# Kernel optimization log

Measured on AMD Instinct MI355X. Metric: run time of the kernel, lower is better.

## Reference

```python
import jax, jax.numpy as jnp
import numpy as np

B, S, D, H = 2, 2048, 512, 8
DK = D // H


def setup_inputs() -> dict:
    key = jax.random.key(0)
    ks = jax.random.split(key, 6)
    q = jax.random.normal(ks[0], (B, S, D), dtype=jnp.float32)
    k = jax.random.normal(ks[1], (B, S, D), dtype=jnp.float32)
    v = jax.random.normal(ks[2], (B, S, D), dtype=jnp.float32)
    mask = jax.random.randint(ks[3], (1, 1, S, S), 0, 2, dtype=jnp.int32)
    # nn.Linear weights [out, in]; scaled like torch default init
    Wq = jax.random.normal(ks[4], (D, D), dtype=jnp.float32) / np.sqrt(D)
    Wo = jax.random.normal(ks[5], (D, D), dtype=jnp.float32) / np.sqrt(D)
    return {"q": q, "k": k, "v": v, "mask": mask, "Wq": Wq, "Wo": Wo}


def _split_heads(x):
    # [B,S,D] -> [B,H,S,DK]
    return x.reshape(B, S, H, DK).transpose(0, 2, 1, 3)


def reference(q, k, v, mask, Wq, Wo):
    # NOTE: original module applies Wq to q, k AND v (faithful to source bug)
    query = _split_heads(q @ Wq.T)
    key_ = _split_heads(k @ Wq.T)
    value = _split_heads(v @ Wq.T)
    scores = jnp.einsum("bhqd,bhkd->bhqk", query, key_) / np.sqrt(DK).astype(np.float32)
    # original uses masked_fill_(mask==0, 1e-09) BEFORE softmax (not -inf)
    scores = jnp.where(mask == 0, jnp.float32(1e-9), scores)
    attn = jax.nn.softmax(scores, axis=-1)  # dropout p=0.0 -> identity
    x = jnp.einsum("bhqk,bhkd->bhqd", attn, value)
    x = x.transpose(0, 2, 1, 3).reshape(B, S, D)
    return x @ Wo.T
```

## Files before the change

kernel.cpp:

```cpp
#include <hip/hip_runtime.h>
#include <hip/hip_bf16.h>
#include <stdint.h>

#define S_LEN 2048
#define D_MOD 512
#define N_H   8
#define D_K   64

typedef short v8s __attribute__((ext_vector_type(8)));
typedef short v4s __attribute__((ext_vector_type(4)));
typedef float v4f __attribute__((ext_vector_type(4)));

__device__ __forceinline__ short f2bf(float f) {
  union { float f; unsigned u; } a; a.f = f;
  unsigned u = a.u;
  u += 0x7fffu + ((u >> 16) & 1u);
  return (short)(u >> 16);
}
__device__ __forceinline__ short f2bfh(float f) {
  union { float f; unsigned u; } a; a.f = f;
  return (short)((a.u + 0x8000u) >> 16);
}
__device__ __forceinline__ float bf2f(short s) {
  union { unsigned u; float f; } x;
  x.u = ((unsigned)(unsigned short)s) << 16;
  return x.f;
}

__device__ __forceinline__ v4f mfma16(v8s a, v8s b, v4f c) {
  return __builtin_amdgcn_mfma_f32_16x16x32_bf16(a, b, c, 0, 0, 0);
}
__device__ __forceinline__ v4f mfma16x16(v4s a, v4s b, v4f c) {
  return __builtin_amdgcn_mfma_f32_16x16x16bf16_1k(a, b, c, 0, 0, 0);
}

__global__ __launch_bounds__(256) void proj_kernel(
    const float* __restrict__ q, const float* __restrict__ k,
    const float* __restrict__ v, const float* __restrict__ Wq,
    const float* __restrict__ Wo, const int* __restrict__ mask,
    short* __restrict__ QP, short* __restrict__ KP, short* __restrict__ VT,
    short* __restrict__ Wob, unsigned long long* __restrict__ mp)
{
  const int z = blockIdx.z;
  const int tid = threadIdx.x;
  if (z == 3) {
    int bid = blockIdx.x * 8 + blockIdx.y;
    if (bid < 256) {
      int id = bid * 256 + tid;
      const int4* m4 = (const int4*)(mask + (size_t)id * 64);
      unsigned long long w = 0ull;
#pragma unroll
      for (int j = 0; j < 16; j++) {
        int4 mv = m4[j];
        w |= (unsigned long long)(mv.x != 0) << (j * 4 + 0);
        w |= (unsigned long long)(mv.y != 0) << (j * 4 + 1);
        w |= (unsigned long long)(mv.z != 0) << (j * 4 + 2);
        w |= (unsigned long long)(mv.w != 0) << (j * 4 + 3);
      }
      mp[id] = w;
    } else {
      unsigned off = (bid - 256) * 256 + tid;
      float4 x = ((const float4*)Wo)[off];
      v4s p; p.x = f2bf(x.x); p.y = f2bf(x.y); p.z = f2bf(x.z); p.w = f2bf(x.w);
      ((v4s*)Wob)[off] = p;
    }
    return;
  }
  const float* __restrict__ A = (z == 0) ? q : ((z == 1) ? k : v);
  const int m0 = blockIdx.x * 64, n0 = blockIdx.y * 64;
  const int wave = tid >> 6, lane = tid & 63;
  const int quad = lane >> 4, l15 = lane & 15;
  const int wm = wave >> 1, wn = wave & 1;
  __shared__ short As[64][72];
  __shared__ short Bs[64][72];
  v4f acc[2][2];
#pragma unroll
  for (int i = 0; i < 2; i++)
#pragma unroll
    for (int j = 0; j < 2; j++) acc[i][j] = (v4f){0.f, 0.f, 0.f, 0.f};

  float4 a4[4], b4[4];
#pragma unroll
  for (int i = 0; i < 4; i++) {
    int fi = tid + i * 256, r = fi >> 4, c = (fi & 15) << 2;
    a4[i] = *(const float4*)&A[(m0 + r) * 512 + c];
    b4[i] = *(const float4*)&Wq[(n0 + r) * 512 + c];
  }

  for (int kk = 0; kk < 512; kk += 64) {
    __syncthreads();
#pragma unroll
    for (int i = 0; i < 4; i++) {
      int fi = tid + i * 256, r = fi >> 4, c = (fi & 15) << 2;
      v4s ap; ap.x = f2bf(a4[i].x); ap.y = f2bf(a4[i].y); ap.z = f2bf(a4[i].z); ap.w = f2bf(a4[i].w);
      *(v4s*)&As[r][c] = ap;
      v4s bp; bp.x = f2bf(b4[i].x); bp.y = f2bf(b4[i].y); bp.z = f2bf(b4[i].z); bp.w = f2bf(b4[i].w);
      *(v4s*)&Bs[r][c] = bp;
    }
    __syncthreads();
    if (kk + 64 < 512) {
#pragma unroll
      for (int i = 0; i < 4; i++) {
        int fi = tid + i * 256, r = fi >> 4, c = (fi & 15) << 2;
        a4[i] = *(const float4*)&A[(m0 + r) * 512 + kk + 64 + c];
        b4[i] = *(const float4*)&Wq[(n0 + r) * 512 + kk + 64 + c];
      }
    }
#pragma unroll
    for (int ms = 0; ms < 2; ms++)
#pragma unroll
      for (int ns = 0; ns < 2; ns++)
#pragma unroll
        for (int ks = 0; ks < 2; ks++) {
          union { v8s v; v4s h2[2]; } a, bb;
          a.h2[0]  = *(const v4s*)&As[wm * 32 + ms * 16 + l15][ks * 32 + quad * 8];
          a.h2[1]  = *(const v4s*)&As[wm * 32 + ms * 16 + l15][ks * 32 + quad * 8 + 4];
          bb.h2[0] = *(const v4s*)&Bs[wn * 32 + ns * 16 + l15][ks * 32 + quad * 8];
          bb.h2[1] = *(const v4s*)&Bs[wn * 32 + ns * 16 + l15][ks * 32 + quad * 8 + 4];
          acc[ms][ns] = mfma16(a.v, bb.v, acc[ms][ns]);
        }
  }
#pragma unroll
  for (int ms = 0; ms < 2; ms++)
#pragma unroll
    for (int ns = 0; ns < 2; ns++) {
      int mb = m0 + wm * 32 + ms * 16 + quad * 4;
      int n  = n0 + wn * 32 + ns * 16 + l15;
      int bI = mb >> 11, s = mb & 2047, hh = n >> 6, dk = n & 63;
      if (z == 2) {
        v4s pv;
        pv.x = f2bf(acc[ms][ns][0]); pv.y = f2bf(acc[ms][ns][1]);
        pv.z = f2bf(acc[ms][ns][2]); pv.w = f2bf(acc[ms][ns][3]);
        *(v4s*)&VT[((bI * N_H + hh) * D_K + dk) * S_LEN + s] = pv;
      } else {
        short* dst = (z == 0) ? QP : KP;
#pragma unroll
        for (int r = 0; r < 4; r++)
          dst[((bI * N_H + hh) * S_LEN + (s + r)) * D_K + dk] = f2bf(acc[ms][ns][r]);
      }
    }
}

__global__ __launch_bounds__(512, 4) void attn_kernel(
    const short* __restrict__ QP, const short* __restrict__ KP,
    const short* __restrict__ VT, const unsigned long long* __restrict__ MP,
    short* __restrict__ XB, float* __restrict__ LP)
{
  const int bx = blockIdx.x;
  const int qt = bx & 15, qu = bx >> 4;
  const int h = blockIdx.y, b = blockIdx.z;
  const int tid = threadIdx.x;
  const int wave = tid >> 6, lane = tid & 63;
  const int quad = lane >> 4, l15 = lane & 15;
  const short* Qh = QP + ((b * N_H + h) * S_LEN) * D_K;
  const short* Kh = KP + ((b * N_H + h) * S_LEN) * D_K;
  const short* Vh = VT + ((b * N_H + h) * D_K) * S_LEN;

  __shared__ short Ks[2][64][72];
  __shared__ short Vs[2][64][72];

  const int qrow = qt * 128 + wave * 16;
  const int srow = tid >> 3;
  const int sc   = (tid & 7) * 8;
  const int ck0  = qu * 512;

  v8s aQ[2];
#pragma unroll
  for (int ks = 0; ks < 2; ks++)
    aQ[ks] = *(const v8s*)&Qh[(qrow + l15) * D_K + ks * 32 + quad * 8];

  const float C1 = 0.18033688011112042f;
  const float C2 = -11.541560327111707f;
  const v4s ONES4 = {16256, 16256, 16256, 16256};
  v4f accX[4], accL = (v4f){0.f, 0.f, 0.f, 0.f};
#pragma unroll
  for (int u = 0; u < 4; u++) accX[u] = (v4f){0.f, 0.f, 0.f, 0.f};

  v8s kr = *(const v8s*)&Kh[(ck0 + srow) * D_K + sc];
  v8s vr = *(const v8s*)&Vh[srow * S_LEN + ck0 + sc];
  *(v8s*)&Ks[0][srow][sc] = kr;
  *(v8s*)&Vs[0][srow][sc] = vr;
  unsigned long long mwc = MP[(qrow + l15) * 32 + qu * 8];
  unsigned long long mwn = 0ull;
  __syncthreads();

  for (int kt = 0; kt < 8; kt++) {
    const int cur = kt & 1;
    if (kt + 1 < 8) {
      const int c1 = ck0 + (kt + 1) * 64;
      kr = *(const v8s*)&Kh[(c1 + srow) * D_K + sc];
      vr = *(const v8s*)&Vh[srow * S_LEN + c1 + sc];
      mwn = MP[(qrow + l15) * 32 + qu * 8 + kt + 1];
    }

    v4s pa[4];
#pragma unroll
    for (int tp = 0; tp < 4; tp++) {
      v8s bK0 = *(const v8s*)&Ks[cur][tp * 16 + l15][quad * 8];
      v8s bK1 = *(const v8s*)&Ks[cur][tp * 16 + l15][32 + quad * 8];
      v4f s = mfma16(bK0, aQ[0], (v4f){0.f, 0.f, 0.f, 0.f});
      s = mfma16(bK1, aQ[1], s);
      unsigned mb = (unsigned)(mwc >> (tp * 16 + quad * 4));
      v4s pk;
#pragma unroll
      for (int r = 0; r < 4; r++) {
        float se = ((mb >> r) & 1u) ? s[r] : 0.0f;
        float p = __builtin_amdgcn_exp2f(fmaf(se, C1, C2));
        pk[r] = f2bfh(p);
      }
      pa[tp] = pk;
    }

#pragma unroll
    for (int u = 0; u < 4; u++) {
      const short* vb_ = &Vs[cur][u * 16 + l15][quad * 4];
#pragma unroll
      for (int tp = 0; tp < 4; tp++) {
        v4s bV = *(const v4s*)&vb_[tp * 16];
        accX[u] = mfma16x16(pa[tp], bV, accX[u]);
      }
    }
#pragma unroll
    for (int tp = 0; tp < 4; tp++)
      accL = mfma16x16(pa[tp], ONES4, accL);

    if (kt + 1 < 8) {
      *(v8s*)&Ks[cur ^ 1][srow][sc] = kr;
      *(v8s*)&Vs[cur ^ 1][srow][sc] = vr;
    }
    __syncthreads();
    mwc = mwn;
  }

  short* xq = XB + (size_t)qu * 2097152u;
#pragma unroll
  for (int u = 0; u < 4; u++)
#pragma unroll
    for (int r = 0; r < 4; r++) {
      int srw = qrow + quad * 4 + r;
      xq[(b * S_LEN + srw) * D_MOD + h * D_K + u * 16 + l15] = f2bf(accX[u][r]);
    }
  if (l15 == 0) {
#pragma unroll
    for (int r = 0; r < 4; r++) {
      int srw = qrow + quad * 4 + r;
      LP[((qu * 2 + b) * S_LEN + srw) * N_H + h] = accL[r];
    }
  }
}

__global__ __launch_bounds__(256) void outproj_kernel(
    const short* __restrict__ XB, const float* __restrict__ LP,
    const short* __restrict__ Wob, float* __restrict__ out)
{
  const int m0 = blockIdx.x * 64, n0 = blockIdx.y * 64;
  const int tid = threadIdx.x;
  const int wave = tid >> 6, lane = tid & 63;
  const int quad = lane >> 4, l15 = lane & 15;
  const int wm = wave >> 1, wn = wave & 1;
  __shared__ short As[64][72];
  __shared__ short Bs[64][72];
  __shared__ float Linv[64][8];

#pragma unroll
  for (int i = 0; i < 2; i++) {
    int e = tid + i * 256;
    int rr = e >> 3, hh = e & 7;
    int s = m0 + rr, bb = s >> 11, sl = s & 2047;
    float l = 0.f;
#pragma unroll
    for (int qu = 0; qu < 4; qu++)
      l += LP[((qu * 2 + bb) * S_LEN + sl) * N_H + hh];
    Linv[rr][hh] = 1.0f / l;
  }

  v4f acc[2][2];
#pragma unroll
  for (int i = 0; i < 2; i++)
#pragma unroll
    for (int j = 0; j < 2; j++) acc[i][j] = (v4f){0.f, 0.f, 0.f, 0.f};

  float af[2][8];
  v8s b8[2];
#pragma unroll
  for (int i = 0; i < 2; i++) {
    int fi = tid + i * 256, r = fi >> 3, c = (fi & 7) << 3;
    size_t base = (size_t)(m0 + r) * 512 + c;
#pragma unroll
    for (int j = 0; j < 8; j++) af[i][j] = 0.f;
#pragma unroll
    for (int qu = 0; qu < 4; qu++) {
      v8s t = *(const v8s*)(XB + (size_t)qu * 2097152u + base);
#pragma unroll
      for (int j = 0; j < 8; j++) af[i][j] += bf2f(t[j]);
    }
    b8[i] = *(const v8s*)&Wob[(n0 + r) * 512 + c];
  }
  __syncthreads();

  for (int kk = 0; kk < 512; kk += 64) {
#pragma unroll
    for (int i = 0; i < 2; i++) {
      int fi = tid + i * 256, r = fi >> 3, c = (fi & 7) << 3;
      float inv = Linv[r][kk >> 6];
      v8s ap;
#pragma unroll
      for (int j = 0; j < 8; j++) ap[j] = f2bf(af[i][j] * inv);
      *(v8s*)&As[r][c] = ap;
      *(v8s*)&Bs[r][c] = b8[i];
    }
    __syncthreads();
    if (kk + 64 < 512) {
#pragma unroll
      for (int i = 0; i < 2; i++) {
        int fi = tid + i * 256, r = fi >> 3, c = (fi & 7) << 3;
        size_t base = (size_t)(m0 + r) * 512 + kk + 64 + c;
#pragma unroll
        for (int j = 0; j < 8; j++) af[i][j] = 0.f;
#pragma unroll
        for (int qu = 0; qu < 4; qu++) {
          v8s t = *(const v8s*)(XB + (size_t)qu * 2097152u + base);
#pragma unroll
          for (int j = 0; j < 8; j++) af[i][j] += bf2f(t[j]);
        }
        b8[i] = *(const v8s*)&Wob[(n0 + r) * 512 + kk + 64 + c];
      }
    }
#pragma unroll
    for (int ms = 0; ms < 2; ms++)
#pragma unroll
      for (int ns = 0; ns < 2; ns++)
#pragma unroll
        for (int ks = 0; ks < 2; ks++) {
          union { v8s v; v4s h2[2]; } a, bb;
          a.h2[0]  = *(const v4s*)&As[wm * 32 + ms * 16 + l15][ks * 32 + quad * 8];
          a.h2[1]  = *(const v4s*)&As[wm * 32 + ms * 16 + l15][ks * 32 + quad * 8 + 4];
          bb.h2[0] = *(const v4s*)&Bs[wn * 32 + ns * 16 + l15][ks * 32 + quad * 8];
          bb.h2[1] = *(const v4s*)&Bs[wn * 32 + ns * 16 + l15][ks * 32 + quad * 8 + 4];
          acc[ms][ns] = mfma16(a.v, bb.v, acc[ms][ns]);
        }
    __syncthreads();
  }
#pragma unroll
  for (int ms = 0; ms < 2; ms++)
#pragma unroll
    for (int ns = 0; ns < 2; ns++) {
      int n = n0 + wn * 32 + ns * 16 + l15;
#pragma unroll
      for (int r = 0; r < 4; r++) {
        int m = m0 + wm * 32 + ms * 16 + quad * 4 + r;
        out[m * 512 + n] = acc[ms][ns][r];
      }
    }
}

extern "C" void kernel_launch(void* const* d_in, const int* in_sizes, int n_in,
                              void* d_out, int out_size, void* d_ws, size_t ws_size,
                              hipStream_t stream) {
  const float* q  = (const float*)d_in[0];
  const float* k  = (const float*)d_in[1];
  const float* v  = (const float*)d_in[2];
  const int* mask = (const int*)d_in[3];
  const float* Wq = (const float*)d_in[4];
  const float* Wo = (const float*)d_in[5];
  float* out = (float*)d_out;
  char* ws = (char*)d_ws;
  short* QP = (short*)(ws);
  short* KP = (short*)(ws + (4u << 20));
  short* VT = (short*)(ws + (8u << 20));
  unsigned long long* MP = (unsigned long long*)(ws + (16u << 20));
  short* Wob = (short*)(ws + (16u << 20) + (512u << 10));
  short* XB = (short*)(ws + (17u << 20));
  float* LP = (float*)(ws + (33u << 20));

  proj_kernel<<<dim3(64, 8, 4), 256, 0, stream>>>(q, k, v, Wq, Wo, mask,
                                                  QP, KP, VT, Wob, MP);
  attn_kernel<<<dim3(64, N_H, 2), 512, 0, stream>>>(QP, KP, VT, MP, XB, LP);
  outproj_kernel<<<dim3(64, 8, 1), 256, 0, stream>>>(XB, LP, Wob, out);
}
```

Baseline: 151.7 us.

## Drop split-K in attention and normalize rows inside the attention kernel

Removes the four-way key split across blocks. Each attention block now walks all 32 key tiles and normalizes its output by the row sum before writing bf16. This removes the partial-sum buffer, the extra XB traffic and the reduction plus rescale work in the output projection. In exchange the attention grid shrinks from 1024 to 256 blocks of 512 threads, which may leave the GPU's compute units underused.

```diff
diff --git a/kernel.cpp b/kernel.cpp
--- a/kernel.cpp
+++ b/kernel.cpp
@@ -144,10 +144,9 @@
 __global__ __launch_bounds__(512, 4) void attn_kernel(
     const short* __restrict__ QP, const short* __restrict__ KP,
     const short* __restrict__ VT, const unsigned long long* __restrict__ MP,
-    short* __restrict__ XB, float* __restrict__ LP)
+    short* __restrict__ XB)
 {
-  const int bx = blockIdx.x;
-  const int qt = bx & 15, qu = bx >> 4;
+  const int qt = blockIdx.x;
   const int h = blockIdx.y, b = blockIdx.z;
   const int tid = threadIdx.x;
   const int wave = tid >> 6, lane = tid & 63;
@@ -162,7 +161,6 @@
   const int qrow = qt * 128 + wave * 16;
   const int srow = tid >> 3;
   const int sc   = (tid & 7) * 8;
-  const int ck0  = qu * 512;
 
   v8s aQ[2];
 #pragma unroll
@@ -176,21 +174,21 @@
 #pragma unroll
   for (int u = 0; u < 4; u++) accX[u] = (v4f){0.f, 0.f, 0.f, 0.f};
 
-  v8s kr = *(const v8s*)&Kh[(ck0 + srow) * D_K + sc];
-  v8s vr = *(const v8s*)&Vh[srow * S_LEN + ck0 + sc];
+  v8s kr = *(const v8s*)&Kh[srow * D_K + sc];
+  v8s vr = *(const v8s*)&Vh[srow * S_LEN + sc];
   *(v8s*)&Ks[0][srow][sc] = kr;
   *(v8s*)&Vs[0][srow][sc] = vr;
-  unsigned long long mwc = MP[(qrow + l15) * 32 + qu * 8];
+  unsigned long long mwc = MP[(qrow + l15) * 32];
   unsigned long long mwn = 0ull;
   __syncthreads();
 
-  for (int kt = 0; kt < 8; kt++) {
+  for (int kt = 0; kt < 32; kt++) {
     const int cur = kt & 1;
-    if (kt + 1 < 8) {
-      const int c1 = ck0 + (kt + 1) * 64;
+    if (kt + 1 < 32) {
+      const int c1 = (kt + 1) * 64;
       kr = *(const v8s*)&Kh[(c1 + srow) * D_K + sc];
       vr = *(const v8s*)&Vh[srow * S_LEN + c1 + sc];
-      mwn = MP[(qrow + l15) * 32 + qu * 8 + kt + 1];
+      mwn = MP[(qrow + l15) * 32 + kt + 1];
     }
 
     v4s pa[4];
@@ -224,7 +222,7 @@
     for (int tp = 0; tp < 4; tp++)
       accL = mfma16x16(pa[tp], ONES4, accL);
 
-    if (kt + 1 < 8) {
+    if (kt + 1 < 32) {
       *(v8s*)&Ks[cur ^ 1][srow][sc] = kr;
       *(v8s*)&Vs[cur ^ 1][srow][sc] = vr;
     }
@@ -232,26 +230,22 @@
     mwc = mwn;
   }
 
-  short* xq = XB + (size_t)qu * 2097152u;
+  v4f linv;
+#pragma unroll
+  for (int r = 0; r < 4; r++) linv[r] = 1.0f / accL[r];
 #pragma unroll
   for (int u = 0; u < 4; u++)
 #pragma unroll
     for (int r = 0; r < 4; r++) {
       int srw = qrow + quad * 4 + r;
-      xq[(b * S_LEN + srw) * D_MOD + h * D_K + u * 16 + l15] = f2bf(accX[u][r]);
-    }
-  if (l15 == 0) {
-#pragma unroll
-    for (int r = 0; r < 4; r++) {
-      int srw = qrow + quad * 4 + r;
-      LP[((qu * 2 + b) * S_LEN + srw) * N_H + h] = accL[r];
-    }
-  }
+      XB[(b * S_LEN + srw) * D_MOD + h * D_K + u * 16 + l15] =
+          f2bf(accX[u][r] * linv[r]);
+    }
 }
 
 __global__ __launch_bounds__(256) void outproj_kernel(
-    const short* __restrict__ XB, const float* __restrict__ LP,
-    const short* __restrict__ Wob, float* __restrict__ out)
+    const short* __restrict__ XB, const short* __restrict__ Wob,
+    float* __restrict__ out)
 {
   const int m0 = blockIdx.x * 64, n0 = blockIdx.y * 64;
   const int tid = threadIdx.x;
@@ -260,19 +254,6 @@
   const int wm = wave >> 1, wn = wave & 1;
   __shared__ short As[64][72];
   __shared__ short Bs[64][72];
-  __shared__ float Linv[64][8];
-
-#pragma unroll
-  for (int i = 0; i < 2; i++) {
-    int e = tid + i * 256;
-    int rr = e >> 3, hh = e & 7;
-    int s = m0 + rr, bb = s >> 11, sl = s & 2047;
-    float l = 0.f;
-#pragma unroll
-    for (int qu = 0; qu < 4; qu++)
-      l += LP[((qu * 2 + bb) * S_LEN + sl) * N_H + hh];
-    Linv[rr][hh] = 1.0f / l;
-  }
 
   v4f acc[2][2];
 #pragma unroll
@@ -280,33 +261,20 @@
 #pragma unroll
     for (int j = 0; j < 2; j++) acc[i][j] = (v4f){0.f, 0.f, 0.f, 0.f};
 
-  float af[2][8];
-  v8s b8[2];
+  v8s a8[2], b8[2];
 #pragma unroll
   for (int i = 0; i < 2; i++) {
     int fi = tid + i * 256, r = fi >> 3, c = (fi & 7) << 3;
-    size_t base = (size_t)(m0 + r) * 512 + c;
-#pragma unroll
-    for (int j = 0; j < 8; j++) af[i][j] = 0.f;
-#pragma unroll
-    for (int qu = 0; qu < 4; qu++) {
-      v8s t = *(const v8s*)(XB + (size_t)qu * 2097152u + base);
-#pragma unroll
-      for (int j = 0; j < 8; j++) af[i][j] += bf2f(t[j]);
-    }
+    a8[i] = *(const v8s*)&XB[(m0 + r) * 512 + c];
     b8[i] = *(const v8s*)&Wob[(n0 + r) * 512 + c];
   }
-  __syncthreads();
 
   for (int kk = 0; kk < 512; kk += 64) {
+    __syncthreads();
 #pragma unroll
     for (int i = 0; i < 2; i++) {
       int fi = tid + i * 256, r = fi >> 3, c = (fi & 7) << 3;
-      float inv = Linv[r][kk >> 6];
-      v8s ap;
-#pragma unroll
-      for (int j = 0; j < 8; j++) ap[j] = f2bf(af[i][j] * inv);
-      *(v8s*)&As[r][c] = ap;
+      *(v8s*)&As[r][c] = a8[i];
       *(v8s*)&Bs[r][c] = b8[i];
     }
     __syncthreads();
@@ -314,15 +282,7 @@
 #pragma unroll
       for (int i = 0; i < 2; i++) {
         int fi = tid + i * 256, r = fi >> 3, c = (fi & 7) << 3;
-        size_t base = (size_t)(m0 + r) * 512 + kk + 64 + c;
-#pragma unroll
-        for (int j = 0; j < 8; j++) af[i][j] = 0.f;
-#pragma unroll
-        for (int qu = 0; qu < 4; qu++) {
-          v8s t = *(const v8s*)(XB + (size_t)qu * 2097152u + base);
-#pragma unroll
-          for (int j = 0; j < 8; j++) af[i][j] += bf2f(t[j]);
-        }
+        a8[i] = *(const v8s*)&XB[(m0 + r) * 512 + kk + 64 + c];
         b8[i] = *(const v8s*)&Wob[(n0 + r) * 512 + kk + 64 + c];
       }
     }
@@ -339,7 +299,6 @@
           bb.h2[1] = *(const v4s*)&Bs[wn * 32 + ns * 16 + l15][ks * 32 + quad * 8 + 4];
           acc[ms][ns] = mfma16(a.v, bb.v, acc[ms][ns]);
         }
-    __syncthreads();
   }
 #pragma unroll
   for (int ms = 0; ms < 2; ms++)
@@ -371,10 +330,9 @@
   unsigned long long* MP = (unsigned long long*)(ws + (16u << 20));
   short* Wob = (short*)(ws + (16u << 20) + (512u << 10));
   short* XB = (short*)(ws + (17u << 20));
-  float* LP = (float*)(ws + (33u << 20));
 
   proj_kernel<<<dim3(64, 8, 4), 256, 0, stream>>>(q, k, v, Wq, Wo, mask,
                                                   QP, KP, VT, Wob, MP);
-  attn_kernel<<<dim3(64, N_H, 2), 512, 0, stream>>>(QP, KP, VT, MP, XB, LP);
-  outproj_kernel<<<dim3(64, 8, 1), 256, 0, stream>>>(XB, LP, Wob, out);
-}
+  attn_kernel<<<dim3(16, N_H, 2), 512, 0, stream>>>(QP, KP, VT, MP, XB);
+  outproj_kernel<<<dim3(64, 8, 1), 256, 0, stream>>>(XB, Wob, out);
+}
```

After: 163.3 us. 7.6% more time.

## Swizzle attention LDS tiles and split partial-sum combine into separate kernel

Applied to the files above, without the earlier changes.

The attention kernel's padded K/V shared tiles are replaced by unpadded 64x64 tiles with an XOR swizzle on the column index, which removes LDS padding and is meant to avoid bank conflicts. The reduction of the four key-split partial outputs and the softmax normalisation move out of the output-projection GEMM into a new elementwise combine kernel. Previously every one of the 8 column blocks re-read all four partial buffers. The GEMM now reads a single normalised bf16 X. This adds a kernel launch and an extra round trip of X through memory.

```diff
diff --git a/kernel.cpp b/kernel.cpp
--- a/kernel.cpp
+++ b/kernel.cpp
@@ -156,12 +156,13 @@
   const short* Kh = KP + ((b * N_H + h) * S_LEN) * D_K;
   const short* Vh = VT + ((b * N_H + h) * D_K) * S_LEN;
 
-  __shared__ short Ks[2][64][72];
-  __shared__ short Vs[2][64][72];
+  __shared__ short SMEM[2][2][64][64];
 
   const int qrow = qt * 128 + wave * 16;
   const int srow = tid >> 3;
-  const int sc   = (tid & 7) * 8;
+  const int sc8  = (tid & 7) * 8;
+  const int scw  = sc8 ^ ((srow & 7) << 3);
+  const int swz  = (l15 & 7) << 3;
   const int ck0  = qu * 512;
 
   v8s aQ[2];
@@ -176,10 +177,10 @@
 #pragma unroll
   for (int u = 0; u < 4; u++) accX[u] = (v4f){0.f, 0.f, 0.f, 0.f};
 
-  v8s kr = *(const v8s*)&Kh[(ck0 + srow) * D_K + sc];
-  v8s vr = *(const v8s*)&Vh[srow * S_LEN + ck0 + sc];
-  *(v8s*)&Ks[0][srow][sc] = kr;
-  *(v8s*)&Vs[0][srow][sc] = vr;
+  v8s kr = *(const v8s*)&Kh[(ck0 + srow) * D_K + sc8];
+  v8s vr = *(const v8s*)&Vh[srow * S_LEN + ck0 + sc8];
+  *(v8s*)&SMEM[0][0][srow][scw] = kr;
+  *(v8s*)&SMEM[0][1][srow][scw] = vr;
   unsigned long long mwc = MP[(qrow + l15) * 32 + qu * 8];
   unsigned long long mwn = 0ull;
   __syncthreads();
@@ -188,16 +189,16 @@
     const int cur = kt & 1;
     if (kt + 1 < 8) {
       const int c1 = ck0 + (kt + 1) * 64;
-      kr = *(const v8s*)&Kh[(c1 + srow) * D_K + sc];
-      vr = *(const v8s*)&Vh[srow * S_LEN + c1 + sc];
+      kr = *(const v8s*)&Kh[(c1 + srow) * D_K + sc8];
+      vr = *(const v8s*)&Vh[srow * S_LEN + c1 + sc8];
       mwn = MP[(qrow + l15) * 32 + qu * 8 + kt + 1];
     }
 
     v4s pa[4];
 #pragma unroll
     for (int tp = 0; tp < 4; tp++) {
-      v8s bK0 = *(const v8s*)&Ks[cur][tp * 16 + l15][quad * 8];
-      v8s bK1 = *(const v8s*)&Ks[cur][tp * 16 + l15][32 + quad * 8];
+      v8s bK0 = *(const v8s*)&SMEM[cur][0][tp * 16 + l15][(quad * 8) ^ swz];
+      v8s bK1 = *(const v8s*)&SMEM[cur][0][tp * 16 + l15][(32 + quad * 8) ^ swz];
       v4f s = mfma16(bK0, aQ[0], (v4f){0.f, 0.f, 0.f, 0.f});
       s = mfma16(bK1, aQ[1], s);
       unsigned mb = (unsigned)(mwc >> (tp * 16 + quad * 4));
@@ -213,10 +214,10 @@
 
 #pragma unroll
     for (int u = 0; u < 4; u++) {
-      const short* vb_ = &Vs[cur][u * 16 + l15][quad * 4];
+      const short* vb_ = &SMEM[cur][1][u * 16 + l15][0];
 #pragma unroll
       for (int tp = 0; tp < 4; tp++) {
-        v4s bV = *(const v4s*)&vb_[tp * 16];
+        v4s bV = *(const v4s*)&vb_[(tp * 16 + quad * 4) ^ swz];
         accX[u] = mfma16x16(pa[tp], bV, accX[u]);
       }
     }
@@ -225,8 +226,8 @@
       accL = mfma16x16(pa[tp], ONES4, accL);
 
     if (kt + 1 < 8) {
-      *(v8s*)&Ks[cur ^ 1][srow][sc] = kr;
-      *(v8s*)&Vs[cur ^ 1][srow][sc] = vr;
+      *(v8s*)&SMEM[cur ^ 1][0][srow][scw] = kr;
+      *(v8s*)&SMEM[cur ^ 1][1][srow][scw] = vr;
     }
     __syncthreads();
     mwc = mwn;
@@ -249,9 +250,39 @@
   }
 }
 
+__global__ __launch_bounds__(256) void combine_kernel(
+    const short* __restrict__ XB, const float* __restrict__ LP,
+    short* __restrict__ X)
+{
+  int g = blockIdx.x * 256 + threadIdx.x;
+  int d8 = g & 63, sf = g >> 6;
+  int b = sf >> 11, s = sf & 2047, hh = d8 >> 3;
+  size_t base = (size_t)g * 8;
+
+  float l = 0.f;
+#pragma unroll
+  for (int qu = 0; qu < 4; qu++)
+    l += LP[((qu * 2 + b) * S_LEN + s) * N_H + hh];
+  float inv = 1.0f / l;
+
+  float acc[8];
+#pragma unroll
+  for (int j = 0; j < 8; j++) acc[j] = 0.f;
+#pragma unroll
+  for (int qu = 0; qu < 4; qu++) {
+    v8s t = *(const v8s*)(XB + (size_t)qu * 2097152u + base);
+#pragma unroll
+    for (int j = 0; j < 8; j++) acc[j] += bf2f(t[j]);
+  }
+  v8s o;
+#pragma unroll
+  for (int j = 0; j < 8; j++) o[j] = f2bf(acc[j] * inv);
+  *(v8s*)(X + base) = o;
+}
+
 __global__ __launch_bounds__(256) void outproj_kernel(
-    const short* __restrict__ XB, const float* __restrict__ LP,
-    const short* __restrict__ Wob, float* __restrict__ out)
+    const short* __restrict__ X, const short* __restrict__ Wob,
+    float* __restrict__ out)
 {
   const int m0 = blockIdx.x * 64, n0 = blockIdx.y * 64;
   const int tid = threadIdx.x;
@@ -260,19 +291,6 @@
   const int wm = wave >> 1, wn = wave & 1;
   __shared__ short As[64][72];
   __shared__ short Bs[64][72];
-  __shared__ float Linv[64][8];
-
-#pragma unroll
-  for (int i = 0; i < 2; i++) {
-    int e = tid + i * 256;
-    int rr = e >> 3, hh = e & 7;
-    int s = m0 + rr, bb = s >> 11, sl = s & 2047;
-    float l = 0.f;
-#pragma unroll
-    for (int qu = 0; qu < 4; qu++)
-      l += LP[((qu * 2 + bb) * S_LEN + sl) * N_H + hh];
-    Linv[rr][hh] = 1.0f / l;
-  }
 
   v4f acc[2][2];
 #pragma unroll
@@ -280,33 +298,20 @@
 #pragma unroll
     for (int j = 0; j < 2; j++) acc[i][j] = (v4f){0.f, 0.f, 0.f, 0.f};
 
-  float af[2][8];
-  v8s b8[2];
+  v8s a8[2], b8[2];
 #pragma unroll
   for (int i = 0; i < 2; i++) {
     int fi = tid + i * 256, r = fi >> 3, c = (fi & 7) << 3;
-    size_t base = (size_t)(m0 + r) * 512 + c;
-#pragma unroll
-    for (int j = 0; j < 8; j++) af[i][j] = 0.f;
-#pragma unroll
-    for (int qu = 0; qu < 4; qu++) {
-      v8s t = *(const v8s*)(XB + (size_t)qu * 2097152u + base);
-#pragma unroll
-      for (int j = 0; j < 8; j++) af[i][j] += bf2f(t[j]);
-    }
+    a8[i] = *(const v8s*)&X[(m0 + r) * 512 + c];
     b8[i] = *(const v8s*)&Wob[(n0 + r) * 512 + c];
   }
-  __syncthreads();
 
   for (int kk = 0; kk < 512; kk += 64) {
+    __syncthreads();
 #pragma unroll
     for (int i = 0; i < 2; i++) {
       int fi = tid + i * 256, r = fi >> 3, c = (fi & 7) << 3;
-      float inv = Linv[r][kk >> 6];
-      v8s ap;
-#pragma unroll
-      for (int j = 0; j < 8; j++) ap[j] = f2bf(af[i][j] * inv);
-      *(v8s*)&As[r][c] = ap;
+      *(v8s*)&As[r][c] = a8[i];
       *(v8s*)&Bs[r][c] = b8[i];
     }
     __syncthreads();
@@ -314,15 +319,7 @@
 #pragma unroll
       for (int i = 0; i < 2; i++) {
         int fi = tid + i * 256, r = fi >> 3, c = (fi & 7) << 3;
-        size_t base = (size_t)(m0 + r) * 512 + kk + 64 + c;
-#pragma unroll
-        for (int j = 0; j < 8; j++) af[i][j] = 0.f;
-#pragma unroll
-        for (int qu = 0; qu < 4; qu++) {
-          v8s t = *(const v8s*)(XB + (size_t)qu * 2097152u + base);
-#pragma unroll
-          for (int j = 0; j < 8; j++) af[i][j] += bf2f(t[j]);
-        }
+        a8[i] = *(const v8s*)&X[(m0 + r) * 512 + kk + 64 + c];
         b8[i] = *(const v8s*)&Wob[(n0 + r) * 512 + kk + 64 + c];
       }
     }
@@ -339,7 +336,6 @@
           bb.h2[1] = *(const v4s*)&Bs[wn * 32 + ns * 16 + l15][ks * 32 + quad * 8 + 4];
           acc[ms][ns] = mfma16(a.v, bb.v, acc[ms][ns]);
         }
-    __syncthreads();
   }
 #pragma unroll
   for (int ms = 0; ms < 2; ms++)
@@ -372,9 +368,11 @@
   short* Wob = (short*)(ws + (16u << 20) + (512u << 10));
   short* XB = (short*)(ws + (17u << 20));
   float* LP = (float*)(ws + (33u << 20));
+  short* X  = (short*)(ws + (34u << 20));
 
   proj_kernel<<<dim3(64, 8, 4), 256, 0, stream>>>(q, k, v, Wq, Wo, mask,
                                                   QP, KP, VT, Wob, MP);
   attn_kernel<<<dim3(64, N_H, 2), 512, 0, stream>>>(QP, KP, VT, MP, XB, LP);
-  outproj_kernel<<<dim3(64, 8, 1), 256, 0, stream>>>(XB, LP, Wob, out);
-}
+  combine_kernel<<<dim3(1024, 1, 1), 256, 0, stream>>>(XB, LP, X);
+  outproj_kernel<<<dim3(64, 8, 1), 256, 0, stream>>>(X, Wob, out);
+}
```

New measurement: 151.8 us. About the same (+0.0%).
